# Kernel optimization log

Hardware: AMD Instinct MI355X
Metric: run time of the kernel (lower is better)

Reference implementation:

```python
import jax, jax.numpy as jnp
import numpy as np

C, W, H = 256, 64, 192
RECORD_LEN = np.array([5, 3, 4, 2, 5, 3, 4, 2], dtype=np.int64)  # sums to 28


def setup_inputs() -> dict:
    key = jax.random.key(0)
    total = int(RECORD_LEN.sum())
    x = jax.random.normal(key, (total, C, W, H), dtype=jnp.float32)
    record_len = jnp.asarray(RECORD_LEN)
    return {"x": x, "record_len": record_len}


def _group_attention(xx):
    # xx: [L, C, W, H] -> per-pixel self-attention over the L agents, d_model = C
    L = xx.shape[0]
    q = xx.reshape(L, C, W * H).transpose(2, 0, 1)          # [N=W*H, L, C]
    score = jnp.einsum('nlc,nmc->nlm', q, q) / jnp.sqrt(jnp.float32(C))
    attn = jax.nn.softmax(score, axis=-1)                    # [N, L, L]
    # original keeps only ego agent (row 0) of the context
    ctx0 = jnp.einsum('nm,nmc->nc', attn[:, 0, :], q)        # [N, C]
    out = ctx0.T.reshape(1, C, W, H)
    attn_maps = attn.transpose(1, 2, 0).reshape(L, L, W, H)
    return out, attn_maps


def reference(x, record_len):
    rl = np.asarray(record_len)  # static ragged lengths
    offsets = np.concatenate([[0], np.cumsum(rl)])
    outs = []
    attn_last = None
    for i in range(len(rl)):  # small fixed number of ragged groups
        xx = x[int(offsets[i]):int(offsets[i + 1])]
        out_i, attn_last = _group_attention(xx)
        outs.append(out_i)
    # matches torch: returns fused ego features per scene + attn of LAST group
    return jnp.concatenate(outs, axis=0), attn_last
```

## Files before the change

kernel.cpp:

```cpp
#include <hip/hip_runtime.h>
#include <math.h>

#define C_DIM 256
#define W_DIM 64
#define H_DIM 192
#define WH (W_DIM * H_DIM)
#define NGROUPS 8
#define NCHUNK 4
#define CCHUNK (C_DIM / NCHUNK)
#define NLOC 64
#define NBLK (WH / NLOC)
#define MAXTRI 15

template <int L, bool WRITE_ATTN>
__device__ __forceinline__ void att_body(
    const float* __restrict__ xg,
    float* __restrict__ out,
    float* __restrict__ attn_out,
    float* __restrict__ lds,
    const int n, const int chunk, const int nl)
{
    constexpr int NTRI = L * (L + 1) / 2;

    float s[NTRI];
#pragma unroll
    for (int i = 0; i < NTRI; ++i) s[i] = 0.0f;

    const int c0 = chunk * CCHUNK;
#pragma unroll 4
    for (int cc = 0; cc < CCHUNK; ++cc) {
        const int c = c0 + cc;
        float v[L];
#pragma unroll
        for (int l = 0; l < L; ++l)
            v[l] = xg[(size_t)(l * C_DIM + c) * WH + n];
        int idx = 0;
#pragma unroll
        for (int l = 0; l < L; ++l)
#pragma unroll
            for (int m = l; m < L; ++m)
                s[idx++] += v[l] * v[m];
    }

#pragma unroll
    for (int i = 0; i < NTRI; ++i)
        lds[i * 256 + chunk * NLOC + nl] = s[i];
    __syncthreads();

    float sf[NTRI];
#pragma unroll
    for (int i = 0; i < NTRI; ++i) {
        float a = lds[i * 256 + nl];
#pragma unroll
        for (int ch = 1; ch < NCHUNK; ++ch)
            a += lds[i * 256 + ch * NLOC + nl];
        sf[i] = a;
    }

    const float scale = 0.0625f;

    float p0[L];
    float mx = -INFINITY;
#pragma unroll
    for (int m = 0; m < L; ++m) {
        p0[m] = sf[m] * scale;
        mx = fmaxf(mx, p0[m]);
    }
    float sum = 0.0f;
#pragma unroll
    for (int m = 0; m < L; ++m) {
        p0[m] = __expf(p0[m] - mx);
        sum += p0[m];
    }
    const float inv = 1.0f / sum;
#pragma unroll
    for (int m = 0; m < L; ++m) p0[m] *= inv;

    if constexpr (WRITE_ATTN) {
        if (chunk == 0) {
            float gm[L][L];
            int idx = 0;
#pragma unroll
            for (int l = 0; l < L; ++l)
#pragma unroll
                for (int m = l; m < L; ++m) {
                    const float v = sf[idx++] * scale;
                    gm[l][m] = v;
                    gm[m][l] = v;
                }
#pragma unroll
            for (int l = 0; l < L; ++l) {
                float mx2 = -INFINITY;
#pragma unroll
                for (int m = 0; m < L; ++m) mx2 = fmaxf(mx2, gm[l][m]);
                float e[L];
                float sm = 0.0f;
#pragma unroll
                for (int m = 0; m < L; ++m) {
                    e[m] = __expf(gm[l][m] - mx2);
                    sm += e[m];
                }
                const float iv = 1.0f / sm;
#pragma unroll
                for (int m = 0; m < L; ++m)
                    __builtin_nontemporal_store(
                        e[m] * iv, &attn_out[(size_t)(l * L + m) * WH + n]);
            }
        }
    }

#pragma unroll 4
    for (int cc = 0; cc < CCHUNK; ++cc) {
        const int c = c0 + cc;
        float acc = 0.0f;
#pragma unroll
        for (int m = 0; m < L; ++m)
            acc += p0[m] * __builtin_nontemporal_load(
                              &xg[(size_t)(m * C_DIM + c) * WH + n]);
        __builtin_nontemporal_store(acc, &out[(size_t)c * WH + n]);
    }
}

__global__ __launch_bounds__(256) void att_fused_kernel(
    const float* __restrict__ x,
    float* __restrict__ out0,
    float* __restrict__ attn)
{
    __shared__ float lds[MAXTRI * 256];

    const int b = blockIdx.x;
    const int g = b / NBLK;
    const int bn = b - g * NBLK;
    const int chunk = threadIdx.x >> 6;
    const int nl = threadIdx.x & 63;
    const int n = bn * NLOC + nl;

    const int offs[NGROUPS] = {0, 5, 8, 12, 14, 19, 22, 26};
    const int lens[NGROUPS] = {5, 3, 4, 2, 5, 3, 4, 2};

    const float* xg = x + (size_t)offs[g] * C_DIM * WH;
    float* og = out0 + (size_t)g * C_DIM * WH;

    switch (lens[g]) {
        case 5: att_body<5, false>(xg, og, nullptr, lds, n, chunk, nl); break;
        case 4: att_body<4, false>(xg, og, nullptr, lds, n, chunk, nl); break;
        case 3: att_body<3, false>(xg, og, nullptr, lds, n, chunk, nl); break;
        case 2:
            if (g == NGROUPS - 1)
                att_body<2, true>(xg, og, attn, lds, n, chunk, nl);
            else
                att_body<2, false>(xg, og, nullptr, lds, n, chunk, nl);
            break;
    }
}

extern "C" void kernel_launch(void* const* d_in, const int* in_sizes, int n_in,
                              void* d_out, int out_size, void* d_ws, size_t ws_size,
                              hipStream_t stream) {
    const float* x = (const float*)d_in[0];
    float* out0 = (float*)d_out;
    float* attn = out0 + (size_t)NGROUPS * C_DIM * WH;

    const dim3 grid(NGROUPS * NBLK);
    const dim3 block(256);
    att_fused_kernel<<<grid, block, 0, stream>>>(x, out0, attn);
}
```

Measured before the change: 532.2 us.

## Cache channel slices in registers to read input once and skip unused score rows

Each thread now loads its slice of channels for all agents into registers once and reuses them for both the score dot products and the weighted context sum, removing the second global read of x. Groups that don't emit attention maps compute only the ego row of scores instead of the full triangle. The block is reshaped to 512 threads with 16 channel chunks over 32 pixels, and attention-map rows are distributed across chunks. This raises register pressure and shortens contiguous access runs per wave.

```diff
diff --git a/kernel.cpp b/kernel.cpp
--- a/kernel.cpp
+++ b/kernel.cpp
@@ -6,11 +6,11 @@
 #define H_DIM 192
 #define WH (W_DIM * H_DIM)
 #define NGROUPS 8
-#define NCHUNK 4
-#define CCHUNK (C_DIM / NCHUNK)
-#define NLOC 64
+#define NCHUNK 16
+#define CCH (C_DIM / NCHUNK)
+#define NLOC 32
 #define NBLK (WH / NLOC)
-#define MAXTRI 15
+#define BLOCK 512
 
 template <int L, bool WRITE_ATTN>
 __device__ __forceinline__ void att_body(
@@ -21,39 +21,52 @@
     const int n, const int chunk, const int nl)
 {
     constexpr int NTRI = L * (L + 1) / 2;
+    constexpr int NACC = WRITE_ATTN ? NTRI : L;
+    static_assert(NACC <= 5, "LDS sized for <=5 accumulators");
 
-    float s[NTRI];
+    const int c0 = chunk * CCH;
+
+    float v[L][CCH];
 #pragma unroll
-    for (int i = 0; i < NTRI; ++i) s[i] = 0.0f;
-
-    const int c0 = chunk * CCHUNK;
-#pragma unroll 4
-    for (int cc = 0; cc < CCHUNK; ++cc) {
-        const int c = c0 + cc;
-        float v[L];
+    for (int cc = 0; cc < CCH; ++cc)
 #pragma unroll
         for (int l = 0; l < L; ++l)
-            v[l] = xg[(size_t)(l * C_DIM + c) * WH + n];
-        int idx = 0;
+            v[l][cc] = xg[(size_t)(l * C_DIM + c0 + cc) * WH + n];
+
+    float s[NACC];
 #pragma unroll
-        for (int l = 0; l < L; ++l)
+    for (int i = 0; i < NACC; ++i) s[i] = 0.0f;
+
+    if constexpr (WRITE_ATTN) {
 #pragma unroll
-            for (int m = l; m < L; ++m)
-                s[idx++] += v[l] * v[m];
+        for (int cc = 0; cc < CCH; ++cc) {
+            int idx = 0;
+#pragma unroll
+            for (int l = 0; l < L; ++l)
+#pragma unroll
+                for (int m = l; m < L; ++m)
+                    s[idx++] += v[l][cc] * v[m][cc];
+        }
+    } else {
+#pragma unroll
+        for (int cc = 0; cc < CCH; ++cc)
+#pragma unroll
+            for (int m = 0; m < L; ++m)
+                s[m] += v[0][cc] * v[m][cc];
     }
 
 #pragma unroll
-    for (int i = 0; i < NTRI; ++i)
-        lds[i * 256 + chunk * NLOC + nl] = s[i];
+    for (int i = 0; i < NACC; ++i)
+        lds[i * BLOCK + chunk * NLOC + nl] = s[i];
     __syncthreads();
 
-    float sf[NTRI];
+    float sf[NACC];
 #pragma unroll
-    for (int i = 0; i < NTRI; ++i) {
-        float a = lds[i * 256 + nl];
+    for (int i = 0; i < NACC; ++i) {
+        float a = 0.0f;
 #pragma unroll
-        for (int ch = 1; ch < NCHUNK; ++ch)
-            a += lds[i * 256 + ch * NLOC + nl];
+        for (int ch = 0; ch < NCHUNK; ++ch)
+            a += lds[i * BLOCK + ch * NLOC + nl];
         sf[i] = a;
     }
 
@@ -77,62 +90,56 @@
     for (int m = 0; m < L; ++m) p0[m] *= inv;
 
     if constexpr (WRITE_ATTN) {
-        if (chunk == 0) {
-            float gm[L][L];
-            int idx = 0;
+        if (chunk < L) {
+            const int r = chunk;
+            float row[L];
 #pragma unroll
-            for (int l = 0; l < L; ++l)
+            for (int m = 0; m < L; ++m) {
+                const int lo = (r < m) ? r : m;
+                const int hi = (r < m) ? m : r;
+                const int idx = lo * L - lo * (lo - 1) / 2 + (hi - lo);
+                row[m] = sf[idx] * scale;
+            }
+            float mx2 = -INFINITY;
 #pragma unroll
-                for (int m = l; m < L; ++m) {
-                    const float v = sf[idx++] * scale;
-                    gm[l][m] = v;
-                    gm[m][l] = v;
-                }
+            for (int m = 0; m < L; ++m) mx2 = fmaxf(mx2, row[m]);
+            float e[L];
+            float sm = 0.0f;
 #pragma unroll
-            for (int l = 0; l < L; ++l) {
-                float mx2 = -INFINITY;
+            for (int m = 0; m < L; ++m) {
+                e[m] = __expf(row[m] - mx2);
+                sm += e[m];
+            }
+            const float iv = 1.0f / sm;
 #pragma unroll
-                for (int m = 0; m < L; ++m) mx2 = fmaxf(mx2, gm[l][m]);
-                float e[L];
-                float sm = 0.0f;
-#pragma unroll
-                for (int m = 0; m < L; ++m) {
-                    e[m] = __expf(gm[l][m] - mx2);
-                    sm += e[m];
-                }
-                const float iv = 1.0f / sm;
-#pragma unroll
-                for (int m = 0; m < L; ++m)
-                    __builtin_nontemporal_store(
-                        e[m] * iv, &attn_out[(size_t)(l * L + m) * WH + n]);
-            }
+            for (int m = 0; m < L; ++m)
+                __builtin_nontemporal_store(
+                    e[m] * iv, &attn_out[(size_t)(r * L + m) * WH + n]);
         }
     }
 
-#pragma unroll 4
-    for (int cc = 0; cc < CCHUNK; ++cc) {
-        const int c = c0 + cc;
+#pragma unroll
+    for (int cc = 0; cc < CCH; ++cc) {
         float acc = 0.0f;
 #pragma unroll
         for (int m = 0; m < L; ++m)
-            acc += p0[m] * __builtin_nontemporal_load(
-                              &xg[(size_t)(m * C_DIM + c) * WH + n]);
-        __builtin_nontemporal_store(acc, &out[(size_t)c * WH + n]);
+            acc += p0[m] * v[m][cc];
+        __builtin_nontemporal_store(acc, &out[(size_t)(c0 + cc) * WH + n]);
     }
 }
 
-__global__ __launch_bounds__(256) void att_fused_kernel(
+__global__ __launch_bounds__(BLOCK, 3) void att_fused_kernel(
     const float* __restrict__ x,
     float* __restrict__ out0,
     float* __restrict__ attn)
 {
-    __shared__ float lds[MAXTRI * 256];
+    __shared__ float lds[5 * BLOCK];
 
     const int b = blockIdx.x;
     const int g = b / NBLK;
     const int bn = b - g * NBLK;
-    const int chunk = threadIdx.x >> 6;
-    const int nl = threadIdx.x & 63;
+    const int chunk = threadIdx.x >> 5;
+    const int nl = threadIdx.x & 31;
     const int n = bn * NLOC + nl;
 
     const int offs[NGROUPS] = {0, 5, 8, 12, 14, 19, 22, 26};
@@ -162,6 +169,6 @@
     float* attn = out0 + (size_t)NGROUPS * C_DIM * WH;
 
     const dim3 grid(NGROUPS * NBLK);
-    const dim3 block(256);
+    const dim3 block(BLOCK);
     att_fused_kernel<<<grid, block, 0, stream>>>(x, out0, attn);
 }
```

Result: faster. 501.2 us (-5.8%).
